# Optimization experiments

Hardware: AMD Instinct MI355X
Metric: run time of the kernel (lower is better)

Reference implementation:

```python
import jax, jax.numpy as jnp
import numpy as np

B, C, H, W_IMG = 4, 4, 512, 512
OUT_CH = 256
POS_NUM = 512
NEG_NUM = 512
M_MARGIN = 0.5
TAU = 0.1
EPS = 1e-8


def setup_inputs() -> dict:
    key = jax.random.key(0)
    k1, k2, k3, k4, k5, k6 = jax.random.split(key, 6)
    d1_fegc = jax.random.normal(k1, (B, C, H, W_IMG), dtype=jnp.float32)
    p_fegc = jax.random.uniform(k2, (B, 1, H, W_IMG), dtype=jnp.float32)
    p_pre = jax.random.uniform(k3, (B, 3, H, W_IMG), dtype=jnp.float32)
    gt = (jax.random.uniform(k4, (B, 1, H, W_IMG)) < 0.5).astype(jnp.float32)
    # parameters of the nn.Linear(in_channel, out_channel)
    W = jax.random.normal(k5, (OUT_CH, C), dtype=jnp.float32) / np.sqrt(C)
    b_fc = jax.random.normal(k6, (OUT_CH,), dtype=jnp.float32) * 0.01
    return {"d1_fegc": d1_fegc, "p_fegc": p_fegc, "p_pre": p_pre, "gt": gt, "W": W, "b_fc": b_fc}


def _sample_idx(mask_flat, key, n):
    # randomized fixed-size sampling of n indices where mask is True
    # (replaces torch.nonzero + randperm with a jit-friendly top-k over random scores)
    score = jnp.where(mask_flat, jax.random.uniform(key, mask_flat.shape), -jnp.inf)
    _, idx = jax.lax.top_k(score, n)
    return idx


def reference(d1_fegc, p_fegc, p_pre, gt, W, b_fc):
    b, c, h, w = d1_fegc.shape
    P = POS_NUM * b
    N = NEG_NUM * b
    # p_overlap channel 3: fegc foreground AND pre argmax-class 0
    fegc_fg = p_fegc[:, 0] >= 0.5                       # [b,h,w]
    pre_cls0 = jnp.argmax(p_pre, axis=1) == 0           # [b,h,w]
    pre_region = fegc_fg & pre_cls0                     # [b,h,w]
    gt_fg = gt[:, 0] > 0.5                              # [b,h,w]
    pos_mask = (pre_region & gt_fg).reshape(-1)         # [b*h*w]
    neg_mask = (pre_region & ~gt_fg).reshape(-1)        # [b*h*w]
    # per-pixel feature vectors from d1_fegc
    feats = d1_fegc.transpose(0, 2, 3, 1).reshape(-1, c)  # [b*h*w, c]
    skey = jax.random.key(42)
    kp, kn = jax.random.split(skey)
    pos_idx = _sample_idx(pos_mask, kp, P)
    neg_idx = _sample_idx(neg_mask, kn, N)
    pts = jnp.concatenate([feats[pos_idx], feats[neg_idx]], axis=0)  # [P+N, c]
    proj = pts @ W.T + b_fc                                           # [P+N, out]
    # F.cosine_similarity with eps=1e-8 norm clamping
    norm = jnp.maximum(jnp.linalg.norm(proj, axis=-1, keepdims=True), EPS)
    normed = proj / norm
    cos_sim = normed @ normed.T                                       # [P+N, P+N]
    T = P + N
    label = jnp.ones((T, T), dtype=cos_sim.dtype)
    label = label.at[:P, P:].set(0.0).at[P:, :P].set(0.0)
    s = cos_sim / TAU
    lam = (1.0 - label) * jnp.square(s) + label * jnp.square(jnp.maximum(M_MARGIN - s, 0.0))
    lam = lam * (1.0 - jnp.eye(T, dtype=lam.dtype))                   # mask self pairs
    denom = jnp.sum(lam != 0).astype(lam.dtype)
    return jnp.sum(lam) / denom
```

## Files before the change

### kernel.cpp

```cpp
#include <hip/hip_runtime.h>
#include <stdint.h>

#define HW       262144u
#define NPIX     1048576u
#define NSEL     2048u
#define NSEG     1024u
#define SEGCAP   16u
#define DENSECAP 3584u

#define OFF_SEG     0u
#define OFF_IDX     262144u
#define OFF_VA      278528u
#define OFF_WA      360448u
#define OFF_PSUM    442368u
#define OFF_PNNZ    446464u

#define TF_ROUND(r) { x0 += x1; x1 = (x1 << (r)) | (x1 >> (32 - (r))); x1 ^= x0; }
__host__ __device__ inline void threefry2x32_(uint32_t k0, uint32_t k1,
                                              uint32_t& x0, uint32_t& x1) {
  uint32_t k2 = k0 ^ k1 ^ 0x1BD11BDAu;
  x0 += k0; x1 += k1;
  TF_ROUND(13) TF_ROUND(15) TF_ROUND(26) TF_ROUND(6)
  x0 += k1; x1 += k2 + 1u;
  TF_ROUND(17) TF_ROUND(29) TF_ROUND(16) TF_ROUND(24)
  x0 += k2; x1 += k0 + 2u;
  TF_ROUND(13) TF_ROUND(15) TF_ROUND(26) TF_ROUND(6)
  x0 += k0; x1 += k1 + 3u;
  TF_ROUND(17) TF_ROUND(29) TF_ROUND(16) TF_ROUND(24)
  x0 += k1; x1 += k2 + 4u;
  TF_ROUND(13) TF_ROUND(15) TF_ROUND(26) TF_ROUND(6)
  x0 += k2; x1 += k0 + 5u;
}

__global__ __launch_bounds__(256) void k_front(
    const float* __restrict__ pfegc, const float* __restrict__ ppre,
    const float* __restrict__ gt,
    uint32_t kp0, uint32_t kp1, uint32_t kn0, uint32_t kn1,
    uint64_t* __restrict__ seg) {
  __shared__ uint32_t cnt2[2];
  int t = threadIdx.x;
  uint32_t b = blockIdx.x;
  if (t < 2) cnt2[t] = 0;
  if (t < 2 * (int)SEGCAP) {
    uint32_t list = (uint32_t)t / SEGCAP, slot = (uint32_t)t % SEGCAP;
    seg[((size_t)list * NSEG + b) * SEGCAP + slot] = 0ull;
  }
  __syncthreads();
  uint32_t base = b * 1024u + (uint32_t)t * 4u;
  float4 pf = *(const float4*)(pfegc + base);
  float pfa[4] = { pf.x, pf.y, pf.z, pf.w };
  bool any = (pf.x >= 0.5f) || (pf.y >= 0.5f) || (pf.z >= 0.5f) || (pf.w >= 0.5f);
  if (any) {
    uint32_t hw = base & (HW - 1u);
    uint32_t bb = base >> 18;
    const float* pp = ppre + (size_t)bb * 3u * HW + hw;
    float4 p0 = *(const float4*)pp;
    float4 p1 = *(const float4*)(pp + HW);
    float4 p2 = *(const float4*)(pp + 2u * HW);
    float4 g4 = *(const float4*)(gt + base);
    float p0a[4] = { p0.x, p0.y, p0.z, p0.w };
    float p1a[4] = { p1.x, p1.y, p1.z, p1.w };
    float p2a[4] = { p2.x, p2.y, p2.z, p2.w };
    float ga[4]  = { g4.x, g4.y, g4.z, g4.w };
    #pragma unroll
    for (int j = 0; j < 4; ++j) {
      if (pfa[j] >= 0.5f && p0a[j] >= p1a[j] && p0a[j] >= p2a[j]) {
        uint32_t i = base + (uint32_t)j;
        bool gfg = ga[j] > 0.5f;
        uint32_t x0 = 0u, x1 = i;
        threefry2x32_(gfg ? kp0 : kn0, gfg ? kp1 : kn1, x0, x1);
        uint32_t r23 = (x0 ^ x1) >> 9;
        if ((r23 >> 18) == 0x1Fu) {
          uint32_t list = gfg ? 0u : 1u;
          uint32_t r = atomicAdd(&cnt2[list], 1u);
          if (r < SEGCAP)
            seg[((size_t)list * NSEG + b) * SEGCAP + r] =
                (1ull << 43) | ((uint64_t)r23 << 20) | (uint64_t)(0xFFFFFu ^ i);
        }
      }
    }
  }
}

__global__ __launch_bounds__(256) void k_sel(
    const uint64_t* __restrict__ seg, uint32_t* __restrict__ idxbuf) {
  __shared__ uint64_t dense[DENSECAP];
  __shared__ uint32_t hist[2048];
  __shared__ uint32_t part[256];
  __shared__ uint32_t cnt, rank, skk;
  __shared__ int gsel;
  __shared__ uint64_t spref;
  int t = threadIdx.x;
  int list = blockIdx.x;
  uint32_t lane = (uint32_t)t & 63u;
  if (t == 0) { cnt = 0; rank = 0; spref = 0ull; skk = NSEL; }
  __syncthreads();
  const uint64_t* sp = seg + (size_t)list * NSEG * SEGCAP;
  for (int it = 0; it < 32; ++it) {
    uint32_t g = (uint32_t)it * 512u + (uint32_t)t * 2u;
    uint64_t k0 = sp[g];
    uint64_t k1 = sp[g + 1u];
    #pragma unroll
    for (int h = 0; h < 2; ++h) {
      uint64_t key = h ? k1 : k0;
      bool v = (key >> 43) != 0ull;
      unsigned long long m = __ballot(v);
      uint32_t bs = 0;
      if (lane == 0) bs = atomicAdd(&cnt, (uint32_t)__popcll(m));
      bs = (uint32_t)__shfl((int)bs, 0, 64);
      if (v) {
        uint32_t s = bs + (uint32_t)__popcll(m & ((1ull << lane) - 1ull));
        if (s < DENSECAP) dense[s] = key;
      }
    }
  }
  __syncthreads();
  uint32_t n = cnt; if (n > DENSECAP) n = DENSECAP;
  for (int r = 0; r < 4; ++r) {
    #pragma unroll
    for (int e = 0; e < 8; ++e) hist[t * 8 + e] = 0;
    __syncthreads();
    int csp = 44 - 11 * r;
    int cs = csp - 11;
    uint64_t pref = spref;
    for (uint32_t j = t; j < n; j += 256) {
      uint64_t key = dense[j];
      if ((key >> csp) == pref)
        atomicAdd(&hist[(uint32_t)(key >> cs) & 0x7FFu], 1u);
    }
    __syncthreads();
    uint32_t ss = 0;
    #pragma unroll
    for (int e = 0; e < 8; ++e) ss += hist[t * 8 + e];
    part[t] = ss;
    __syncthreads();
    for (int off = 1; off < 256; off <<= 1) {
      uint32_t x = part[t];
      uint32_t y = (t + off < 256) ? part[t + off] : 0u;
      __syncthreads();
      part[t] = x + y;
      __syncthreads();
    }
    uint32_t k = skk;
    if (part[t] >= k && (t == 255 || part[t + 1] < k)) gsel = t;
    __syncthreads();
    if (t == 0) {
      int g = gsel;
      uint32_t cum = (g < 255) ? part[g + 1] : 0u;
      int d = g * 8;
      for (int e = g * 8 + 7; e >= g * 8; --e) {
        uint32_t he = hist[e];
        if (cum + he >= k) { d = e; break; }
        cum += he;
      }
      skk = k - cum;
      spref = (pref << 11) | (uint64_t)(uint32_t)d;
    }
    __syncthreads();
  }
  uint64_t thr = spref;
  uint32_t niter = (n + 255u) >> 8;
  for (uint32_t it2 = 0; it2 < niter; ++it2) {
    uint32_t j = it2 * 256u + (uint32_t)t;
    uint64_t key = 0ull;
    bool v = false;
    if (j < n) { key = dense[j]; v = key >= thr; }
    unsigned long long m = __ballot(v);
    uint32_t bs = 0;
    if (lane == 0) bs = atomicAdd(&rank, (uint32_t)__popcll(m));
    bs = (uint32_t)__shfl((int)bs, 0, 64);
    if (v) {
      uint32_t s = bs + (uint32_t)__popcll(m & ((1ull << lane) - 1ull));
      if (s < NSEL)
        idxbuf[(uint32_t)list * NSEL + s] = 0xFFFFFu ^ (uint32_t)(key & 0xFFFFFu);
    }
  }
}

__global__ __launch_bounds__(256) void k_proj(
    const uint32_t* __restrict__ idxbuf, const float* __restrict__ Wm,
    const float* __restrict__ bfc, const float* __restrict__ d1,
    float* __restrict__ va, float* __restrict__ wa) {
  __shared__ float sG[25];
  __shared__ float sGw[4][25];
  int t = threadIdx.x;
  {
    float4 wr = *(const float4*)(Wm + t * 4);
    float av[5] = { wr.x, wr.y, wr.z, wr.w, bfc[t] };
    int lane = t & 63, wvi = t >> 6;
    #pragma unroll
    for (int p = 0; p < 5; ++p)
      #pragma unroll
      for (int q = p; q < 5; ++q) {
        float g = av[p] * av[q];
        #pragma unroll
        for (int off = 32; off > 0; off >>= 1)
          g += __shfl_xor(g, off, 64);
        if (lane == 0) sGw[wvi][p * 5 + q] = g;
      }
  }
  __syncthreads();
  if (t < 25) {
    int p = t / 5, q = t % 5;
    int pp = p < q ? p : q, qq = p < q ? q : p;
    sG[t] = sGw[0][pp * 5 + qq] + sGw[1][pp * 5 + qq]
          + sGw[2][pp * 5 + qq] + sGw[3][pp * 5 + qq];
  }
  __syncthreads();
  uint32_t tg = blockIdx.x * 256u + (uint32_t)t;
  uint32_t idx = idxbuf[tg] & (NPIX - 1u);
  uint32_t hw = idx & (HW - 1u);
  uint32_t bb = idx >> 18;
  const float* f = d1 + ((size_t)bb << 20) + hw;
  float y[5] = { f[0], f[HW], f[2u * HW], f[3u * HW], 1.0f };
  float z[5]; float n2 = 0.f;
  #pragma unroll
  for (int p = 0; p < 5; ++p) {
    float acc = 0.f;
    #pragma unroll
    for (int q = 0; q < 5; ++q) acc += sG[p * 5 + q] * y[q];
    z[p] = acc; n2 += acc * y[p];
  }
  n2 = fmaxf(n2, 0.f);
  float inv = 1.0f / fmaxf(sqrtf(n2), 1e-8f);
  uint32_t s5 = tg * 5u;
  #pragma unroll
  for (int p = 0; p < 5; ++p) {
    va[s5 + p] = y[p] * inv;
    wa[s5 + p] = z[p] * inv;
  }
}

__global__ __launch_bounds__(256) void k_pair(
    const float* __restrict__ va, const float* __restrict__ wa,
    float* __restrict__ psum, uint32_t* __restrict__ pnnz) {
  __shared__ float sv[128 * 5], sw[128 * 5];
  int i0 = blockIdx.x * 128, j0 = blockIdx.y * 128;
  int t = threadIdx.x;
  for (int u = t; u < 640; u += 256) { sv[u] = va[i0 * 5 + u]; sw[u] = wa[j0 * 5 + u]; }
  __syncthreads();
  int ty = t >> 4, tx = t & 15;
  float rv[8][5], rw[8][5];
  #pragma unroll
  for (int a = 0; a < 8; ++a)
    #pragma unroll
    for (int p = 0; p < 5; ++p) {
      rv[a][p] = sv[(ty * 8 + a) * 5 + p];
      rw[a][p] = sw[(tx * 8 + a) * 5 + p];
    }
  float lsum = 0.f; uint32_t lnz = 0;
  #pragma unroll
  for (int a = 0; a < 8; ++a) {
    int gi = i0 + ty * 8 + a;
    #pragma unroll
    for (int q = 0; q < 8; ++q) {
      int gj = j0 + tx * 8 + q;
      float c = rv[a][0]*rw[q][0] + rv[a][1]*rw[q][1] + rv[a][2]*rw[q][2]
              + rv[a][3]*rw[q][3] + rv[a][4]*rw[q][4];
      float s = c * 10.0f;
      if (gi != gj) {
        if (((gi ^ gj) & 2048) == 0) {
          float m = fmaxf(0.5f - s, 0.f);
          lsum += m * m;
          lnz += (m > 0.f) ? 1u : 0u;
        } else {
          lsum += s * s;
          lnz += (s != 0.f) ? 1u : 0u;
        }
      }
    }
  }
  __shared__ float rs[256];
  __shared__ uint32_t rn[256];
  rs[t] = lsum; rn[t] = lnz;
  __syncthreads();
  for (int off = 128; off > 0; off >>= 1) {
    if (t < off) { rs[t] += rs[t + off]; rn[t] += rn[t + off]; }
    __syncthreads();
  }
  if (t == 0) {
    int bid = blockIdx.y * gridDim.x + blockIdx.x;
    psum[bid] = rs[0];
    pnnz[bid] = rn[0];
  }
}

__global__ __launch_bounds__(256) void k_final(const float* __restrict__ psum,
                                               const uint32_t* __restrict__ pnnz,
                                               float* __restrict__ out) {
  __shared__ float rs[256];
  __shared__ uint32_t rn[256];
  int t = threadIdx.x;
  float s = 0.f; uint32_t nz = 0;
  for (int j = t; j < 1024; j += 256) { s += psum[j]; nz += pnnz[j]; }
  rs[t] = s; rn[t] = nz;
  __syncthreads();
  for (int off = 128; off > 0; off >>= 1) {
    if (t < off) { rs[t] += rs[t + off]; rn[t] += rn[t + off]; }
    __syncthreads();
  }
  if (t == 0) out[0] = rs[0] / (float)rn[0];
}

extern "C" void kernel_launch(void* const* d_in, const int* in_sizes, int n_in,
                              void* d_out, int out_size, void* d_ws, size_t ws_size,
                              hipStream_t stream) {
  (void)in_sizes; (void)n_in; (void)out_size; (void)ws_size;
  const float* d1    = (const float*)d_in[0];
  const float* pfegc = (const float*)d_in[1];
  const float* ppre  = (const float*)d_in[2];
  const float* gt    = (const float*)d_in[3];
  const float* W     = (const float*)d_in[4];
  const float* bfc   = (const float*)d_in[5];
  float* out = (float*)d_out;

  uint8_t* base = (uint8_t*)d_ws;
  uint64_t* seg    = (uint64_t*)(base + OFF_SEG);
  uint32_t* idxbuf = (uint32_t*)(base + OFF_IDX);
  float*    va     = (float*)(base + OFF_VA);
  float*    wa     = (float*)(base + OFF_WA);
  float*    psum   = (float*)(base + OFF_PSUM);
  uint32_t* pnnz   = (uint32_t*)(base + OFF_PNNZ);

  uint32_t kp0 = 0u, kp1 = 0u; threefry2x32_(0u, 42u, kp0, kp1);
  uint32_t kn0 = 0u, kn1 = 1u; threefry2x32_(0u, 42u, kn0, kn1);

  k_front<<<NSEG, 256, 0, stream>>>(pfegc, ppre, gt, kp0, kp1, kn0, kn1, seg);
  k_sel<<<2, 256, 0, stream>>>(seg, idxbuf);
  k_proj<<<16, 256, 0, stream>>>(idxbuf, W, bfc, d1, va, wa);
  k_pair<<<dim3(32, 32), 256, 0, stream>>>(va, wa, psum, pnnz);
  k_final<<<1, 256, 0, stream>>>(psum, pnnz, out);
}
```

Baseline: 130.7 us.

## Fuse selection with projection and fold final reduction into pair kernel

Merges the top-k selection kernel with the projection kernel, so the selected indices stay in shared memory and never make a round trip through global memory. The last finishing block of the pair kernel, found through atomic done-counters, now does the final reduction. This removes two kernel launches. In exchange, projection runs on only 2 blocks instead of 16, and done-counters are added that k_front must reset on every call.

```diff
diff --git a/kernel.cpp b/kernel.cpp
--- a/kernel.cpp
+++ b/kernel.cpp
@@ -9,11 +9,11 @@
 #define DENSECAP 3584u
 
 #define OFF_SEG     0u
-#define OFF_IDX     262144u
-#define OFF_VA      278528u
-#define OFF_WA      360448u
-#define OFF_PSUM    442368u
-#define OFF_PNNZ    446464u
+#define OFF_VA      262144u
+#define OFF_WA      344064u
+#define OFF_PSUM    425984u
+#define OFF_PNNZ    430080u
+#define OFF_DONE    434176u
 
 #define TF_ROUND(r) { x0 += x1; x1 = (x1 << (r)) | (x1 >> (32 - (r))); x1 ^= x0; }
 __host__ __device__ inline void threefry2x32_(uint32_t k0, uint32_t k1,
@@ -36,11 +36,12 @@
     const float* __restrict__ pfegc, const float* __restrict__ ppre,
     const float* __restrict__ gt,
     uint32_t kp0, uint32_t kp1, uint32_t kn0, uint32_t kn1,
-    uint64_t* __restrict__ seg) {
+    uint64_t* __restrict__ seg, uint32_t* __restrict__ done) {
   __shared__ uint32_t cnt2[2];
   int t = threadIdx.x;
   uint32_t b = blockIdx.x;
   if (t < 2) cnt2[t] = 0;
+  if (b == 0 && t < 33) done[t] = 0u;
   if (t < 2 * (int)SEGCAP) {
     uint32_t list = (uint32_t)t / SEGCAP, slot = (uint32_t)t % SEGCAP;
     seg[((size_t)list * NSEG + b) * SEGCAP + slot] = 0ull;
@@ -82,18 +83,45 @@
   }
 }
 
-__global__ __launch_bounds__(256) void k_sel(
-    const uint64_t* __restrict__ seg, uint32_t* __restrict__ idxbuf) {
+__global__ __launch_bounds__(256) void k_selproj(
+    const uint64_t* __restrict__ seg,
+    const float* __restrict__ Wm, const float* __restrict__ bfc,
+    const float* __restrict__ d1,
+    float* __restrict__ va, float* __restrict__ wa) {
   __shared__ uint64_t dense[DENSECAP];
   __shared__ uint32_t hist[2048];
   __shared__ uint32_t part[256];
   __shared__ uint32_t cnt, rank, skk;
   __shared__ int gsel;
   __shared__ uint64_t spref;
+  __shared__ float sG[25];
+  __shared__ float sGw[4][25];
   int t = threadIdx.x;
   int list = blockIdx.x;
   uint32_t lane = (uint32_t)t & 63u;
+  {
+    float4 wr = *(const float4*)(Wm + t * 4);
+    float av[5] = { wr.x, wr.y, wr.z, wr.w, bfc[t] };
+    int wvi = t >> 6;
+    #pragma unroll
+    for (int p = 0; p < 5; ++p)
+      #pragma unroll
+      for (int q = p; q < 5; ++q) {
+        float g = av[p] * av[q];
+        #pragma unroll
+        for (int off = 32; off > 0; off >>= 1)
+          g += __shfl_xor(g, off, 64);
+        if (lane == 0) sGw[wvi][p * 5 + q] = g;
+      }
+  }
   if (t == 0) { cnt = 0; rank = 0; spref = 0ull; skk = NSEL; }
+  __syncthreads();
+  if (t < 25) {
+    int p = t / 5, q = t % 5;
+    int pp = p < q ? p : q, qq = p < q ? q : p;
+    sG[t] = sGw[0][pp * 5 + qq] + sGw[1][pp * 5 + qq]
+          + sGw[2][pp * 5 + qq] + sGw[3][pp * 5 + qq];
+  }
   __syncthreads();
   const uint64_t* sp = seg + (size_t)list * NSEG * SEGCAP;
   for (int it = 0; it < 32; ++it) {
@@ -171,70 +199,43 @@
     bs = (uint32_t)__shfl((int)bs, 0, 64);
     if (v) {
       uint32_t s = bs + (uint32_t)__popcll(m & ((1ull << lane) - 1ull));
-      if (s < NSEL)
-        idxbuf[(uint32_t)list * NSEL + s] = 0xFFFFFu ^ (uint32_t)(key & 0xFFFFFu);
-    }
-  }
-}
-
-__global__ __launch_bounds__(256) void k_proj(
-    const uint32_t* __restrict__ idxbuf, const float* __restrict__ Wm,
-    const float* __restrict__ bfc, const float* __restrict__ d1,
-    float* __restrict__ va, float* __restrict__ wa) {
-  __shared__ float sG[25];
-  __shared__ float sGw[4][25];
-  int t = threadIdx.x;
-  {
-    float4 wr = *(const float4*)(Wm + t * 4);
-    float av[5] = { wr.x, wr.y, wr.z, wr.w, bfc[t] };
-    int lane = t & 63, wvi = t >> 6;
-    #pragma unroll
-    for (int p = 0; p < 5; ++p)
+      if (s < NSEL) hist[s] = 0xFFFFFu ^ (uint32_t)(key & 0xFFFFFu);
+    }
+  }
+  __syncthreads();
+  for (uint32_t j = t; j < NSEL; j += 256) {
+    uint32_t idx = hist[j] & (NPIX - 1u);
+    uint32_t hw = idx & (HW - 1u);
+    uint32_t bb = idx >> 18;
+    const float* f = d1 + ((size_t)bb << 20) + hw;
+    float y[5] = { f[0], f[HW], f[2u * HW], f[3u * HW], 1.0f };
+    float z[5]; float n2 = 0.f;
+    #pragma unroll
+    for (int p = 0; p < 5; ++p) {
+      float acc = 0.f;
       #pragma unroll
-      for (int q = p; q < 5; ++q) {
-        float g = av[p] * av[q];
-        #pragma unroll
-        for (int off = 32; off > 0; off >>= 1)
-          g += __shfl_xor(g, off, 64);
-        if (lane == 0) sGw[wvi][p * 5 + q] = g;
-      }
-  }
-  __syncthreads();
-  if (t < 25) {
-    int p = t / 5, q = t % 5;
-    int pp = p < q ? p : q, qq = p < q ? q : p;
-    sG[t] = sGw[0][pp * 5 + qq] + sGw[1][pp * 5 + qq]
-          + sGw[2][pp * 5 + qq] + sGw[3][pp * 5 + qq];
-  }
-  __syncthreads();
-  uint32_t tg = blockIdx.x * 256u + (uint32_t)t;
-  uint32_t idx = idxbuf[tg] & (NPIX - 1u);
-  uint32_t hw = idx & (HW - 1u);
-  uint32_t bb = idx >> 18;
-  const float* f = d1 + ((size_t)bb << 20) + hw;
-  float y[5] = { f[0], f[HW], f[2u * HW], f[3u * HW], 1.0f };
-  float z[5]; float n2 = 0.f;
-  #pragma unroll
-  for (int p = 0; p < 5; ++p) {
-    float acc = 0.f;
-    #pragma unroll
-    for (int q = 0; q < 5; ++q) acc += sG[p * 5 + q] * y[q];
-    z[p] = acc; n2 += acc * y[p];
-  }
-  n2 = fmaxf(n2, 0.f);
-  float inv = 1.0f / fmaxf(sqrtf(n2), 1e-8f);
-  uint32_t s5 = tg * 5u;
-  #pragma unroll
-  for (int p = 0; p < 5; ++p) {
-    va[s5 + p] = y[p] * inv;
-    wa[s5 + p] = z[p] * inv;
+      for (int q = 0; q < 5; ++q) acc += sG[p * 5 + q] * y[q];
+      z[p] = acc; n2 += acc * y[p];
+    }
+    n2 = fmaxf(n2, 0.f);
+    float inv = 1.0f / fmaxf(sqrtf(n2), 1e-8f);
+    uint32_t s5 = ((uint32_t)list * NSEL + j) * 5u;
+    #pragma unroll
+    for (int p = 0; p < 5; ++p) {
+      va[s5 + p] = y[p] * inv;
+      wa[s5 + p] = z[p] * inv;
+    }
   }
 }
 
 __global__ __launch_bounds__(256) void k_pair(
     const float* __restrict__ va, const float* __restrict__ wa,
-    float* __restrict__ psum, uint32_t* __restrict__ pnnz) {
+    float* __restrict__ psum, uint32_t* __restrict__ pnnz,
+    uint32_t* __restrict__ done, float* __restrict__ out) {
   __shared__ float sv[128 * 5], sw[128 * 5];
+  __shared__ float rs[256];
+  __shared__ uint32_t rn[256];
+  __shared__ int islast;
   int i0 = blockIdx.x * 128, j0 = blockIdx.y * 128;
   int t = threadIdx.x;
   for (int u = t; u < 640; u += 256) { sv[u] = va[i0 * 5 + u]; sw[u] = wa[j0 * 5 + u]; }
@@ -270,36 +271,41 @@
       }
     }
   }
-  __shared__ float rs[256];
-  __shared__ uint32_t rn[256];
   rs[t] = lsum; rn[t] = lnz;
   __syncthreads();
   for (int off = 128; off > 0; off >>= 1) {
     if (t < off) { rs[t] += rs[t + off]; rn[t] += rn[t + off]; }
     __syncthreads();
   }
+  int bid = blockIdx.y * gridDim.x + blockIdx.x;
   if (t == 0) {
-    int bid = blockIdx.y * gridDim.x + blockIdx.x;
-    psum[bid] = rs[0];
-    pnnz[bid] = rn[0];
-  }
-}
-
-__global__ __launch_bounds__(256) void k_final(const float* __restrict__ psum,
-                                               const uint32_t* __restrict__ pnnz,
-                                               float* __restrict__ out) {
-  __shared__ float rs[256];
-  __shared__ uint32_t rn[256];
-  int t = threadIdx.x;
-  float s = 0.f; uint32_t nz = 0;
-  for (int j = t; j < 1024; j += 256) { s += psum[j]; nz += pnnz[j]; }
-  rs[t] = s; rn[t] = nz;
-  __syncthreads();
-  for (int off = 128; off > 0; off >>= 1) {
-    if (t < off) { rs[t] += rs[t + off]; rn[t] += rn[t + off]; }
-    __syncthreads();
-  }
-  if (t == 0) out[0] = rs[0] / (float)rn[0];
+    atomicExch(&psum[bid], rs[0]);
+    atomicExch(&pnnz[bid], rn[0]);
+    __threadfence();
+    int last = 0;
+    uint32_t o1 = atomicAdd(&done[blockIdx.y], 1u);
+    if (o1 == 31u) {
+      uint32_t o2 = atomicAdd(&done[32], 1u);
+      last = (o2 == 31u);
+    }
+    islast = last;
+  }
+  __syncthreads();
+  if (islast) {
+    float s = 0.f; uint32_t nz = 0;
+    for (int j = t; j < 1024; j += 256) {
+      s += atomicAdd(&psum[j], 0.0f);
+      nz += atomicAdd(&pnnz[j], 0u);
+    }
+    __syncthreads();
+    rs[t] = s; rn[t] = nz;
+    __syncthreads();
+    for (int off = 128; off > 0; off >>= 1) {
+      if (t < off) { rs[t] += rs[t + off]; rn[t] += rn[t + off]; }
+      __syncthreads();
+    }
+    if (t == 0) out[0] = rs[0] / (float)rn[0];
+  }
 }
 
 extern "C" void kernel_launch(void* const* d_in, const int* in_sizes, int n_in,
@@ -315,19 +321,17 @@
   float* out = (float*)d_out;
 
   uint8_t* base = (uint8_t*)d_ws;
-  uint64_t* seg    = (uint64_t*)(base + OFF_SEG);
-  uint32_t* idxbuf = (uint32_t*)(base + OFF_IDX);
-  float*    va     = (float*)(base + OFF_VA);
-  float*    wa     = (float*)(base + OFF_WA);
-  float*    psum   = (float*)(base + OFF_PSUM);
-  uint32_t* pnnz   = (uint32_t*)(base + OFF_PNNZ);
+  uint64_t* seg  = (uint64_t*)(base + OFF_SEG);
+  float*    va   = (float*)(base + OFF_VA);
+  float*    wa   = (float*)(base + OFF_WA);
+  float*    psum = (float*)(base + OFF_PSUM);
+  uint32_t* pnnz = (uint32_t*)(base + OFF_PNNZ);
+  uint32_t* done = (uint32_t*)(base + OFF_DONE);
 
   uint32_t kp0 = 0u, kp1 = 0u; threefry2x32_(0u, 42u, kp0, kp1);
   uint32_t kn0 = 0u, kn1 = 1u; threefry2x32_(0u, 42u, kn0, kn1);
 
-  k_front<<<NSEG, 256, 0, stream>>>(pfegc, ppre, gt, kp0, kp1, kn0, kn1, seg);
-  k_sel<<<2, 256, 0, stream>>>(seg, idxbuf);
-  k_proj<<<16, 256, 0, stream>>>(idxbuf, W, bfc, d1, va, wa);
-  k_pair<<<dim3(32, 32), 256, 0, stream>>>(va, wa, psum, pnnz);
-  k_final<<<1, 256, 0, stream>>>(psum, pnnz, out);
-}
+  k_front<<<NSEG, 256, 0, stream>>>(pfegc, ppre, gt, kp0, kp1, kn0, kn1, seg, done);
+  k_selproj<<<2, 256, 0, stream>>>(seg, W, bfc, d1, va, wa);
+  k_pair<<<dim3(32, 32), 256, 0, stream>>>(va, wa, psum, pnnz, done, out);
+}
```

After: 155.9 us. +19.3%, slower.

## Fuse final reduction into pair kernel and replace atomic compaction with prefix scan

Applied to the files above, without the earlier changes.

The final reduction kernel is removed. The last k_pair block, detected through two-level atomic completion counters that k_front resets, now reduces the partial sums and writes the output, which saves one kernel launch. Separately, k_sel's stream compaction swaps per-wave ballot plus shared atomics for a per-thread count, a block-wide prefix scan, and a second ordered read pass. This adds global atomics, fences and a second read of the segment buffer in exchange for fewer launches and less atomic contention.

```diff
diff --git a/kernel.cpp b/kernel.cpp
--- a/kernel.cpp
+++ b/kernel.cpp
@@ -14,6 +14,7 @@
 #define OFF_WA      360448u
 #define OFF_PSUM    442368u
 #define OFF_PNNZ    446464u
+#define OFF_DONE    450560u
 
 #define TF_ROUND(r) { x0 += x1; x1 = (x1 << (r)) | (x1 >> (32 - (r))); x1 ^= x0; }
 __host__ __device__ inline void threefry2x32_(uint32_t k0, uint32_t k1,
@@ -36,11 +37,12 @@
     const float* __restrict__ pfegc, const float* __restrict__ ppre,
     const float* __restrict__ gt,
     uint32_t kp0, uint32_t kp1, uint32_t kn0, uint32_t kn1,
-    uint64_t* __restrict__ seg) {
+    uint64_t* __restrict__ seg, uint32_t* __restrict__ done) {
   __shared__ uint32_t cnt2[2];
   int t = threadIdx.x;
   uint32_t b = blockIdx.x;
   if (t < 2) cnt2[t] = 0;
+  if (b == 0 && t < 33) done[t] = 0u;
   if (t < 2 * (int)SEGCAP) {
     uint32_t list = (uint32_t)t / SEGCAP, slot = (uint32_t)t % SEGCAP;
     seg[((size_t)list * NSEG + b) * SEGCAP + slot] = 0ull;
@@ -87,35 +89,43 @@
   __shared__ uint64_t dense[DENSECAP];
   __shared__ uint32_t hist[2048];
   __shared__ uint32_t part[256];
-  __shared__ uint32_t cnt, rank, skk;
+  __shared__ uint32_t skk, rank, ntot;
   __shared__ int gsel;
   __shared__ uint64_t spref;
   int t = threadIdx.x;
   int list = blockIdx.x;
   uint32_t lane = (uint32_t)t & 63u;
-  if (t == 0) { cnt = 0; rank = 0; spref = 0ull; skk = NSEL; }
-  __syncthreads();
+  if (t == 0) { spref = 0ull; skk = NSEL; rank = 0; }
   const uint64_t* sp = seg + (size_t)list * NSEG * SEGCAP;
+  uint32_t c = 0;
+  #pragma unroll
   for (int it = 0; it < 32; ++it) {
     uint32_t g = (uint32_t)it * 512u + (uint32_t)t * 2u;
     uint64_t k0 = sp[g];
     uint64_t k1 = sp[g + 1u];
-    #pragma unroll
-    for (int h = 0; h < 2; ++h) {
-      uint64_t key = h ? k1 : k0;
-      bool v = (key >> 43) != 0ull;
-      unsigned long long m = __ballot(v);
-      uint32_t bs = 0;
-      if (lane == 0) bs = atomicAdd(&cnt, (uint32_t)__popcll(m));
-      bs = (uint32_t)__shfl((int)bs, 0, 64);
-      if (v) {
-        uint32_t s = bs + (uint32_t)__popcll(m & ((1ull << lane) - 1ull));
-        if (s < DENSECAP) dense[s] = key;
-      }
-    }
-  }
-  __syncthreads();
-  uint32_t n = cnt; if (n > DENSECAP) n = DENSECAP;
+    c += (uint32_t)(k0 >> 43) + (uint32_t)(k1 >> 43);
+  }
+  part[t] = c;
+  __syncthreads();
+  for (int off = 1; off < 256; off <<= 1) {
+    uint32_t x = part[t];
+    uint32_t add = (t >= off) ? part[t - off] : 0u;
+    __syncthreads();
+    part[t] = x + add;
+    __syncthreads();
+  }
+  uint32_t wbase = part[t] - c;
+  if (t == 255) ntot = part[255];
+  #pragma unroll
+  for (int it = 0; it < 32; ++it) {
+    uint32_t g = (uint32_t)it * 512u + (uint32_t)t * 2u;
+    uint64_t k0 = sp[g];
+    uint64_t k1 = sp[g + 1u];
+    if (k0 >> 43) { if (wbase < DENSECAP) dense[wbase] = k0; ++wbase; }
+    if (k1 >> 43) { if (wbase < DENSECAP) dense[wbase] = k1; ++wbase; }
+  }
+  __syncthreads();
+  uint32_t n = ntot; if (n > DENSECAP) n = DENSECAP;
   for (int r = 0; r < 4; ++r) {
     #pragma unroll
     for (int e = 0; e < 8; ++e) hist[t * 8 + e] = 0;
@@ -233,8 +243,12 @@
 
 __global__ __launch_bounds__(256) void k_pair(
     const float* __restrict__ va, const float* __restrict__ wa,
-    float* __restrict__ psum, uint32_t* __restrict__ pnnz) {
+    float* __restrict__ psum, uint32_t* __restrict__ pnnz,
+    uint32_t* __restrict__ done, float* __restrict__ out) {
   __shared__ float sv[128 * 5], sw[128 * 5];
+  __shared__ float rs[256];
+  __shared__ uint32_t rn[256];
+  __shared__ int islast;
   int i0 = blockIdx.x * 128, j0 = blockIdx.y * 128;
   int t = threadIdx.x;
   for (int u = t; u < 640; u += 256) { sv[u] = va[i0 * 5 + u]; sw[u] = wa[j0 * 5 + u]; }
@@ -270,36 +284,41 @@
       }
     }
   }
-  __shared__ float rs[256];
-  __shared__ uint32_t rn[256];
   rs[t] = lsum; rn[t] = lnz;
   __syncthreads();
   for (int off = 128; off > 0; off >>= 1) {
     if (t < off) { rs[t] += rs[t + off]; rn[t] += rn[t + off]; }
     __syncthreads();
   }
+  int bid = blockIdx.y * gridDim.x + blockIdx.x;
   if (t == 0) {
-    int bid = blockIdx.y * gridDim.x + blockIdx.x;
-    psum[bid] = rs[0];
-    pnnz[bid] = rn[0];
-  }
-}
-
-__global__ __launch_bounds__(256) void k_final(const float* __restrict__ psum,
-                                               const uint32_t* __restrict__ pnnz,
-                                               float* __restrict__ out) {
-  __shared__ float rs[256];
-  __shared__ uint32_t rn[256];
-  int t = threadIdx.x;
-  float s = 0.f; uint32_t nz = 0;
-  for (int j = t; j < 1024; j += 256) { s += psum[j]; nz += pnnz[j]; }
-  rs[t] = s; rn[t] = nz;
-  __syncthreads();
-  for (int off = 128; off > 0; off >>= 1) {
-    if (t < off) { rs[t] += rs[t + off]; rn[t] += rn[t + off]; }
-    __syncthreads();
-  }
-  if (t == 0) out[0] = rs[0] / (float)rn[0];
+    atomicExch(&psum[bid], rs[0]);
+    atomicExch(&pnnz[bid], rn[0]);
+    __threadfence();
+    int last = 0;
+    uint32_t o1 = atomicAdd(&done[blockIdx.y], 1u);
+    if (o1 == 31u) {
+      uint32_t o2 = atomicAdd(&done[32], 1u);
+      last = (o2 == 31u);
+    }
+    islast = last;
+  }
+  __syncthreads();
+  if (islast) {
+    float s = 0.f; uint32_t nz = 0;
+    for (int j = t; j < 1024; j += 256) {
+      s += atomicAdd(&psum[j], 0.0f);
+      nz += atomicAdd(&pnnz[j], 0u);
+    }
+    __syncthreads();
+    rs[t] = s; rn[t] = nz;
+    __syncthreads();
+    for (int off = 128; off > 0; off >>= 1) {
+      if (t < off) { rs[t] += rs[t + off]; rn[t] += rn[t + off]; }
+      __syncthreads();
+    }
+    if (t == 0) out[0] = rs[0] / (float)rn[0];
+  }
 }
 
 extern "C" void kernel_launch(void* const* d_in, const int* in_sizes, int n_in,
@@ -321,13 +340,13 @@
   float*    wa     = (float*)(base + OFF_WA);
   float*    psum   = (float*)(base + OFF_PSUM);
   uint32_t* pnnz   = (uint32_t*)(base + OFF_PNNZ);
+  uint32_t* done   = (uint32_t*)(base + OFF_DONE);
 
   uint32_t kp0 = 0u, kp1 = 0u; threefry2x32_(0u, 42u, kp0, kp1);
   uint32_t kn0 = 0u, kn1 = 1u; threefry2x32_(0u, 42u, kn0, kn1);
 
-  k_front<<<NSEG, 256, 0, stream>>>(pfegc, ppre, gt, kp0, kp1, kn0, kn1, seg);
+  k_front<<<NSEG, 256, 0, stream>>>(pfegc, ppre, gt, kp0, kp1, kn0, kn1, seg, done);
   k_sel<<<2, 256, 0, stream>>>(seg, idxbuf);
   k_proj<<<16, 256, 0, stream>>>(idxbuf, W, bfc, d1, va, wa);
-  k_pair<<<dim3(32, 32), 256, 0, stream>>>(va, wa, psum, pnnz);
-  k_final<<<1, 256, 0, stream>>>(psum, pnnz, out);
-}
+  k_pair<<<dim3(32, 32), 256, 0, stream>>>(va, wa, psum, pnnz, done, out);
+}
```

New measurement: 138.0 us. 5.5% more time.
